# Kernel optimization log

Hardware: AMD Instinct MI355X
Metric: run time of the kernel (lower is better)

The kernel has to match this reference:

```python
import jax, jax.numpy as jnp
import numpy as np

NUM_USERS = 100000
NUM_MOVIES = 50000
NUM_NODES = NUM_USERS + NUM_MOVIES
EMB_DIM = 64
N_LAYERS = 3
N_EDGES = 4000000


def setup_inputs() -> dict:
    key = jax.random.key(0)
    k_e, k_w = jax.random.split(key)
    edge_index = jax.random.randint(k_e, (2, N_EDGES), 0, NUM_NODES, dtype=jnp.int64 if jax.config.jax_enable_x64 else jnp.int32)
    emb_weight = jax.random.normal(k_w, (NUM_NODES, EMB_DIM), dtype=jnp.float32)
    return {"edge_index": edge_index, "emb_weight": emb_weight}


def reference(edge_index, emb_weight):
    row, col = edge_index[0], edge_index[1]
    num_nodes = emb_weight.shape[0]
    # degree of each node as a scatter-add destination (col)
    deg = jax.ops.segment_sum(jnp.ones_like(col, dtype=emb_weight.dtype), col,
                              num_segments=num_nodes)
    deg_inv_sqrt = jnp.where(deg > 0, jax.lax.rsqrt(jnp.maximum(deg, 1.0)), 0.0)
    deg_inv_sqrt = jnp.where(deg > 0, deg ** -0.5, 0.0)
    norm = deg_inv_sqrt[row] * deg_inv_sqrt[col]  # [E]

    embs = emb_weight
    acc = emb_weight  # running sum for the final mean over layers
    for _ in range(N_LAYERS):
        msgs = norm[:, None] * embs[row]  # [E, D] gather + scale
        embs = jax.ops.segment_sum(msgs, col, num_segments=num_nodes)  # [N, D]
        acc = acc + embs
    return acc / (N_LAYERS + 1)
```

## Files before the change

### kernel.cpp

```cpp
#include <hip/hip_runtime.h>
#include <hip/hip_fp16.h>

#define D 64
constexpr int TPB = 256;
constexpr int PTPB = 512;
constexpr int CTPB = 512;
constexpr int VSHIFT = 8;
constexpr int VNODES = 1 << VSHIFT;
constexpr int CHUNK = 8192;
constexpr int CAP = 8192;
constexpr int MAXBUK = 640;
typedef unsigned short u16;

__device__ inline unsigned h2pack(float a, float b) {
    unsigned lo = __half_as_ushort(__float2half_rn(a));
    unsigned hi = __half_as_ushort(__float2half_rn(b));
    return lo | (hi << 16);
}

__global__ void fuseAB_kernel(const int* __restrict__ row, const int* __restrict__ col,
                              int* __restrict__ gcnt, unsigned* __restrict__ tmp,
                              int E, int NBUK) {
    __shared__ int h[MAXBUK];
    __shared__ int cur[MAXBUK];
    int t = threadIdx.x, blk = blockIdx.x;
    for (int b = t; b < NBUK; b += PTPB) h[b] = 0;
    __syncthreads();
    int base = blk * CHUNK;
    int n = min(CHUNK, E - base);
    for (int i = t; i < n; i += PTPB)
        atomicAdd(&h[col[base + i] >> VSHIFT], 1);
    __syncthreads();
    for (int b = t; b < NBUK; b += PTPB) {
        int c = h[b];
        cur[b] = (c > 0) ? atomicAdd(&gcnt[b], c) : 0;
    }
    __syncthreads();
    for (int i = t; i < n; i += PTPB) {
        int c = col[base + i];
        int b = c >> VSHIFT;
        int p = atomicAdd(&cur[b], 1);
        if (p < CAP)
            tmp[(size_t)b * CAP + p] =
                ((unsigned)(c & (VNODES - 1)) << 18) | (unsigned)row[base + i];
    }
}

__global__ void bscan_kernel(const int* __restrict__ gcnt, int* __restrict__ bExcl, int nb) {
    __shared__ int s[1024];
    int t = threadIdx.x;
    int v = (t < nb) ? gcnt[t] : 0;
    s[t] = v;
    __syncthreads();
    for (int off = 1; off < 1024; off <<= 1) {
        int x = (t >= off) ? s[t - off] : 0;
        __syncthreads();
        s[t] += x;
        __syncthreads();
    }
    if (t < nb) bExcl[t] = s[t] - v;
}

__global__ void passC_kernel(const unsigned* __restrict__ tmp, const int* __restrict__ gcnt,
                             const int* __restrict__ bExcl,
                             int* __restrict__ row_ptr, float* __restrict__ dis,
                             int* __restrict__ srow, int N, int E) {
    __shared__ int cnt[VNODES], sc[VNODES], cur[VNODES];
    int b = blockIdx.x, t = threadIdx.x;
    int nodeBase = b << VSHIFT;
    if (t < VNODES) cnt[t] = 0;
    __syncthreads();
    int m = min(gcnt[b], CAP);
    const unsigned* __restrict__ tb = tmp + (size_t)b * CAP;
    for (int i = t; i < m; i += CTPB)
        atomicAdd(&cnt[tb[i] >> 18], 1);
    __syncthreads();
    if (t < VNODES) sc[t] = cnt[t];
    __syncthreads();
    for (int off = 1; off < VNODES; off <<= 1) {
        int i = (t + 1) * (off << 1) - 1;
        if (i < VNODES) sc[i] += sc[i - off];
        __syncthreads();
    }
    if (t == 0) sc[VNODES - 1] = 0;
    __syncthreads();
    for (int off = VNODES / 2; off >= 1; off >>= 1) {
        int i = (t + 1) * (off << 1) - 1;
        if (i < VNODES) { int x = sc[i - off]; sc[i - off] = sc[i]; sc[i] += x; }
        __syncthreads();
    }
    int gbase = bExcl[b];
    if (t < VNODES) {
        int rp = gbase + sc[t];
        cur[t] = rp;
        int node = nodeBase + t;
        if (node < N) {
            row_ptr[node] = rp;
            int d = cnt[t];
            dis[node] = (d > 0) ? rsqrtf((float)d) : 0.0f;
        }
    }
    if (b == 0 && t == 0) row_ptr[N] = E;
    __syncthreads();
    for (int i = t; i < m; i += CTPB) {
        unsigned pk = tb[i];
        int p = atomicAdd(&cur[pk >> 18], 1);
        srow[p] = (int)(pk & 0x3FFFFu);
    }
}

__global__ void z0_kernel(const float4* __restrict__ emb4, const float* __restrict__ dis,
                          unsigned* __restrict__ A, unsigned* __restrict__ B, int N) {
    int total = N * 16;
    int stride = gridDim.x * blockDim.x;
    uint2* __restrict__ A2 = (uint2*)A;
    for (int i = blockIdx.x * blockDim.x + threadIdx.x; i < total; i += stride) {
        int node = i >> 4;
        float dv = dis[node];
        float4 x = emb4[i];
        uint2 o;
        o.x = h2pack(dv * x.x, dv * x.y);
        o.y = h2pack(dv * x.z, dv * x.w);
        A2[i] = o;
    }
    if (blockIdx.x == 0 && threadIdx.x < 32) {
        A[(size_t)N * 32 + threadIdx.x] = 0;
        B[(size_t)N * 32 + threadIdx.x] = 0;
    }
}

#define ACC8(u) do { \
    a0 += __half2float(__ushort_as_half((u16)((u).x & 0xffff))); \
    a1 += __half2float(__ushort_as_half((u16)((u).x >> 16)));    \
    a2 += __half2float(__ushort_as_half((u16)((u).y & 0xffff))); \
    a3 += __half2float(__ushort_as_half((u16)((u).y >> 16)));    \
    a4 += __half2float(__ushort_as_half((u16)((u).z & 0xffff))); \
    a5 += __half2float(__ushort_as_half((u16)((u).z >> 16)));    \
    a6 += __half2float(__ushort_as_half((u16)((u).w & 0xffff))); \
    a7 += __half2float(__ushort_as_half((u16)((u).w >> 16)));    \
} while (0)

template <int MODE, bool WRITE_DST>
__global__ void spmm_kernel(const int* __restrict__ row_ptr, const int* __restrict__ srow,
                            const float* __restrict__ dis,
                            const unsigned* __restrict__ src, unsigned* __restrict__ dst,
                            float2* __restrict__ out2, const float2* __restrict__ emb2,
                            int N) {
    int wave = (blockIdx.x * blockDim.x + threadIdx.x) >> 6;
    int lane = threadIdx.x & 63;
    int half = lane >> 5;
    int sub  = lane & 31;
    int node = 2 * wave + half;
    if (node >= N) return;
    int start = row_ptr[node];
    int end   = row_ptr[node + 1];
    int hb = half << 5;
    int rg = sub >> 3;
    int q  = sub & 7;
    const uint4* __restrict__ s4 = (const uint4*)src;
    float a0 = 0, a1 = 0, a2 = 0, a3 = 0, a4 = 0, a5 = 0, a6 = 0, a7 = 0;
    for (int base = start; base < end; base += 32) {
        int mye = base + sub;
        int rr = (mye < end) ? srow[mye] : 0;
        int cnt = end - base;
        int r0 = __shfl(rr, hb +  0 + rg);
        int r1 = __shfl(rr, hb +  4 + rg);
        int r2 = __shfl(rr, hb +  8 + rg);
        int r3 = __shfl(rr, hb + 12 + rg);
        int r4 = __shfl(rr, hb + 16 + rg);
        int r5 = __shfl(rr, hb + 20 + rg);
        int r6 = __shfl(rr, hb + 24 + rg);
        int r7 = __shfl(rr, hb + 28 + rg);
        r0 = ( 0 + rg < cnt) ? r0 : N;
        r1 = ( 4 + rg < cnt) ? r1 : N;
        r2 = ( 8 + rg < cnt) ? r2 : N;
        r3 = (12 + rg < cnt) ? r3 : N;
        r4 = (16 + rg < cnt) ? r4 : N;
        r5 = (20 + rg < cnt) ? r5 : N;
        r6 = (24 + rg < cnt) ? r6 : N;
        r7 = (28 + rg < cnt) ? r7 : N;
        uint4 u0 = s4[(size_t)r0 * 8 + q];
        uint4 u1 = s4[(size_t)r1 * 8 + q];
        uint4 u2 = s4[(size_t)r2 * 8 + q];
        uint4 u3 = s4[(size_t)r3 * 8 + q];
        uint4 u4 = s4[(size_t)r4 * 8 + q];
        uint4 u5 = s4[(size_t)r5 * 8 + q];
        uint4 u6 = s4[(size_t)r6 * 8 + q];
        uint4 u7 = s4[(size_t)r7 * 8 + q];
        ACC8(u0); ACC8(u1); ACC8(u2); ACC8(u3);
        ACC8(u4); ACC8(u5); ACC8(u6); ACC8(u7);
    }
    a0 += __shfl_xor(a0, 8);  a1 += __shfl_xor(a1, 8);
    a2 += __shfl_xor(a2, 8);  a3 += __shfl_xor(a3, 8);
    a4 += __shfl_xor(a4, 8);  a5 += __shfl_xor(a5, 8);
    a6 += __shfl_xor(a6, 8);  a7 += __shfl_xor(a7, 8);
    a0 += __shfl_xor(a0, 16); a1 += __shfl_xor(a1, 16);
    a2 += __shfl_xor(a2, 16); a3 += __shfl_xor(a3, 16);
    a4 += __shfl_xor(a4, 16); a5 += __shfl_xor(a5, 16);
    a6 += __shfl_xor(a6, 16); a7 += __shfl_xor(a7, 16);
    if (rg != 0) return;
    float dc = dis[node];
    float e0 = dc * a0, e1 = dc * a1, e2 = dc * a2, e3 = dc * a3;
    float e4 = dc * a4, e5 = dc * a5, e6 = dc * a6, e7 = dc * a7;
    if (WRITE_DST) {
        uint4 pk;
        pk.x = h2pack(dc * e0, dc * e1);
        pk.y = h2pack(dc * e2, dc * e3);
        pk.z = h2pack(dc * e4, dc * e5);
        pk.w = h2pack(dc * e6, dc * e7);
        ((uint4*)dst)[(size_t)node * 8 + q] = pk;
    }
    size_t fo = (size_t)node * 16 + q * 2;
    float4* __restrict__ o4 = (float4*)out2;
    float4 c0, c1;
    if (MODE == 0) {
        const float4* __restrict__ e4p = (const float4*)emb2;
        c0 = e4p[fo]; c1 = e4p[fo + 1];
        c0.x += e0; c0.y += e1; c0.z += e2; c0.w += e3;
        c1.x += e4; c1.y += e5; c1.z += e6; c1.w += e7;
    } else if (MODE == 1) {
        c0 = o4[fo]; c1 = o4[fo + 1];
        c0.x += e0; c0.y += e1; c0.z += e2; c0.w += e3;
        c1.x += e4; c1.y += e5; c1.z += e6; c1.w += e7;
    } else {
        c0 = o4[fo]; c1 = o4[fo + 1];
        c0.x = (c0.x + e0) * 0.25f; c0.y = (c0.y + e1) * 0.25f;
        c0.z = (c0.z + e2) * 0.25f; c0.w = (c0.w + e3) * 0.25f;
        c1.x = (c1.x + e4) * 0.25f; c1.y = (c1.y + e5) * 0.25f;
        c1.z = (c1.z + e6) * 0.25f; c1.w = (c1.w + e7) * 0.25f;
    }
    o4[fo] = c0; o4[fo + 1] = c1;
}

extern "C" void kernel_launch(void* const* d_in, const int* in_sizes, int n_in,
                              void* d_out, int out_size, void* d_ws, size_t ws_size,
                              hipStream_t stream) {
    const int* edge = (const int*)d_in[0];
    const float* emb = (const float*)d_in[1];
    const int E = in_sizes[0] / 2;
    const int N = in_sizes[1] / D;
    float2* out2 = (float2*)d_out;

    const int* row = edge;
    const int* col = edge + E;

    const int NBLK = (E + CHUNK - 1) / CHUNK;
    const int NBUK = (N + VNODES - 1) >> VSHIFT;

    size_t zrow = (size_t)(N + 1) * 32;
    size_t tsz  = (size_t)NBUK * CAP;
    size_t bsz  = (tsz > zrow) ? tsz : zrow;
    unsigned* A       = (unsigned*)d_ws;
    unsigned* B       = A + zrow;
    unsigned* tmp     = B;
    int*      srow    = (int*)(B + bsz);
    int*      row_ptr = srow + E;
    float*    dis     = (float*)(row_ptr + N + 1);
    int*      gcnt    = (int*)(dis + N);
    int*      bExcl   = gcnt + NBUK;

    const int spmm_blocks = (((N + 1) / 2) * 64 + TPB - 1) / TPB;

    hipMemsetAsync(gcnt, 0, (size_t)NBUK * sizeof(int), stream);
    fuseAB_kernel<<<NBLK, PTPB, 0, stream>>>(row, col, gcnt, tmp, E, NBUK);
    bscan_kernel<<<1, 1024, 0, stream>>>(gcnt, bExcl, NBUK);
    passC_kernel<<<NBUK, CTPB, 0, stream>>>(tmp, gcnt, bExcl, row_ptr, dis,
                                            srow, N, E);
    z0_kernel<<<2048, TPB, 0, stream>>>((const float4*)emb, dis, A, B, N);

    spmm_kernel<0, true><<<spmm_blocks, TPB, 0, stream>>>(row_ptr, srow, dis, A, B,
                                                          out2, (const float2*)emb, N);
    spmm_kernel<1, true><<<spmm_blocks, TPB, 0, stream>>>(row_ptr, srow, dis, B, A,
                                                          out2, (const float2*)emb, N);
    spmm_kernel<2, false><<<spmm_blocks, TPB, 0, stream>>>(row_ptr, srow, dis, A, nullptr,
                                                           out2, (const float2*)emb, N);
}
```

Before: 445.8 us.

## Fuse embedding prescale into CSR build pass and pad global bucket counters

```diff
diff --git a/kernel.cpp b/kernel.cpp
--- a/kernel.cpp
+++ b/kernel.cpp
@@ -7,9 +7,10 @@
 constexpr int CTPB = 512;
 constexpr int VSHIFT = 8;
 constexpr int VNODES = 1 << VSHIFT;
-constexpr int CHUNK = 8192;
+constexpr int CHUNK = 16384;
 constexpr int CAP = 8192;
 constexpr int MAXBUK = 640;
+constexpr int GPAD = 16;
 typedef unsigned short u16;
 
 __device__ inline unsigned h2pack(float a, float b) {
@@ -33,7 +34,7 @@
     __syncthreads();
     for (int b = t; b < NBUK; b += PTPB) {
         int c = h[b];
-        cur[b] = (c > 0) ? atomicAdd(&gcnt[b], c) : 0;
+        cur[b] = (c > 0) ? atomicAdd(&gcnt[b * GPAD], c) : 0;
     }
     __syncthreads();
     for (int i = t; i < n; i += PTPB) {
@@ -49,7 +50,7 @@
 __global__ void bscan_kernel(const int* __restrict__ gcnt, int* __restrict__ bExcl, int nb) {
     __shared__ int s[1024];
     int t = threadIdx.x;
-    int v = (t < nb) ? gcnt[t] : 0;
+    int v = (t < nb) ? gcnt[t * GPAD] : 0;
     s[t] = v;
     __syncthreads();
     for (int off = 1; off < 1024; off <<= 1) {
@@ -64,13 +65,16 @@
 __global__ void passC_kernel(const unsigned* __restrict__ tmp, const int* __restrict__ gcnt,
                              const int* __restrict__ bExcl,
                              int* __restrict__ row_ptr, float* __restrict__ dis,
-                             int* __restrict__ srow, int N, int E) {
+                             int* __restrict__ srow,
+                             const float2* __restrict__ emb2, unsigned* __restrict__ A,
+                             int N, int E) {
     __shared__ int cnt[VNODES], sc[VNODES], cur[VNODES];
     int b = blockIdx.x, t = threadIdx.x;
     int nodeBase = b << VSHIFT;
     if (t < VNODES) cnt[t] = 0;
-    __syncthreads();
-    int m = min(gcnt[b], CAP);
+    if (b == 0 && t < 32) A[(size_t)N * 32 + t] = 0;
+    __syncthreads();
+    int m = min(gcnt[b * GPAD], CAP);
     const unsigned* __restrict__ tb = tmp + (size_t)b * CAP;
     for (int i = t; i < m; i += CTPB)
         atomicAdd(&cnt[tb[i] >> 18], 1);
@@ -107,25 +111,16 @@
         int p = atomicAdd(&cur[pk >> 18], 1);
         srow[p] = (int)(pk & 0x3FFFFu);
     }
-}
-
-__global__ void z0_kernel(const float4* __restrict__ emb4, const float* __restrict__ dis,
-                          unsigned* __restrict__ A, unsigned* __restrict__ B, int N) {
-    int total = N * 16;
-    int stride = gridDim.x * blockDim.x;
-    uint2* __restrict__ A2 = (uint2*)A;
-    for (int i = blockIdx.x * blockDim.x + threadIdx.x; i < total; i += stride) {
-        int node = i >> 4;
-        float dv = dis[node];
-        float4 x = emb4[i];
-        uint2 o;
-        o.x = h2pack(dv * x.x, dv * x.y);
-        o.y = h2pack(dv * x.z, dv * x.w);
-        A2[i] = o;
-    }
-    if (blockIdx.x == 0 && threadIdx.x < 32) {
-        A[(size_t)N * 32 + threadIdx.x] = 0;
-        B[(size_t)N * 32 + threadIdx.x] = 0;
+    for (int i = t; i < (VNODES << 5); i += CTPB) {
+        int k = i >> 5;
+        int node = nodeBase + k;
+        if (node < N) {
+            int d = cnt[k];
+            float dv = (d > 0) ? rsqrtf((float)d) : 0.0f;
+            size_t o = (size_t)node * 32 + (i & 31);
+            float2 x = emb2[o];
+            A[o] = h2pack(dv * x.x, dv * x.y);
+        }
     }
 }
 
@@ -146,6 +141,8 @@
                             const unsigned* __restrict__ src, unsigned* __restrict__ dst,
                             float2* __restrict__ out2, const float2* __restrict__ emb2,
                             int N) {
+    if (WRITE_DST && blockIdx.x == 0 && threadIdx.x < 32)
+        dst[(size_t)N * 32 + threadIdx.x] = 0;
     int wave = (blockIdx.x * blockDim.x + threadIdx.x) >> 6;
     int lane = threadIdx.x & 63;
     int half = lane >> 5;
@@ -257,16 +254,15 @@
     int*      row_ptr = srow + E;
     float*    dis     = (float*)(row_ptr + N + 1);
     int*      gcnt    = (int*)(dis + N);
-    int*      bExcl   = gcnt + NBUK;
+    int*      bExcl   = gcnt + NBUK * GPAD;
 
     const int spmm_blocks = (((N + 1) / 2) * 64 + TPB - 1) / TPB;
 
-    hipMemsetAsync(gcnt, 0, (size_t)NBUK * sizeof(int), stream);
+    hipMemsetAsync(gcnt, 0, (size_t)NBUK * GPAD * sizeof(int), stream);
     fuseAB_kernel<<<NBLK, PTPB, 0, stream>>>(row, col, gcnt, tmp, E, NBUK);
     bscan_kernel<<<1, 1024, 0, stream>>>(gcnt, bExcl, NBUK);
     passC_kernel<<<NBUK, CTPB, 0, stream>>>(tmp, gcnt, bExcl, row_ptr, dis,
-                                            srow, N, E);
-    z0_kernel<<<2048, TPB, 0, stream>>>((const float4*)emb, dis, A, B, N);
+                                            srow, (const float2*)emb, A, N, E);
 
     spmm_kernel<0, true><<<spmm_blocks, TPB, 0, stream>>>(row_ptr, srow, dis, A, B,
                                                           out2, (const float2*)emb, N);
```

After: 450.1 us. No clear change (+1.0%).
